# Optimization experiments

Measured on AMD Instinct MI355X. Metric: run time of the kernel, lower is better.

## Reference

```python
import jax, jax.numpy as jnp
import numpy as np

HIDDEN = 1024
NUM_HEADS = 16
HEAD_SIZE = HIDDEN // NUM_HEADS  # 64
SQ, SK, B = 256, 1024, 8


def setup_inputs() -> dict:
    key = jax.random.key(0)
    ks = jax.random.split(key, 8)
    s = 0.02
    return {
        "x": jax.random.normal(ks[0], (SQ, B, HIDDEN), jnp.float32),
        "memory": jax.random.normal(ks[1], (SK, B, HIDDEN), jnp.float32),
        "Wq": jax.random.normal(ks[2], (HIDDEN, HIDDEN), jnp.float32) * s,
        "bq": jax.random.normal(ks[3], (HIDDEN,), jnp.float32) * s,
        "Wkv": jax.random.normal(ks[4], (2 * HIDDEN, HIDDEN), jnp.float32) * s,
        "bkv": jax.random.normal(ks[5], (2 * HIDDEN,), jnp.float32) * s,
        "Wd": jax.random.normal(ks[6], (HIDDEN, HIDDEN), jnp.float32) * s,
        "bd": jax.random.normal(ks[7], (HIDDEN,), jnp.float32) * s,
    }


def reference(x, memory, Wq, bq, Wkv, bkv, Wd, bd):
    # x: (Sq, B, E), memory: (Sk, B, E)  -- sequence-first layout
    Sq, Bb, E = x.shape
    Sk = memory.shape[0]
    H, Dh = NUM_HEADS, HEAD_SIZE

    q = x @ Wq.T + bq            # (Sq, B, E)
    kv = memory @ Wkv.T + bkv    # (Sk, B, 2E)

    # view (..., H, Dh) then composite permute (1,3,0,2):
    # NOTE: the original module's chained permutes put tensors in
    # (batch, head_size, seq, num_heads) layout, so the score matmul
    # contracts over num_heads and head_size acts as the head axis.
    q = q.reshape(Sq, Bb, H, Dh).transpose((1, 3, 0, 2))          # (B, Dh, Sq, H)
    kv = kv.reshape(Sk, Bb, H, 2 * Dh)
    k = kv[..., :Dh].transpose((1, 3, 0, 2))                       # (B, Dh, Sk, H)
    v = kv[..., Dh:].transpose((1, 3, 0, 2))                       # (B, Dh, Sk, H)

    scale = 1.0 / np.sqrt(float(Dh)).astype(np.float32)
    scores = jnp.einsum('bdqh,bdkh->bdqk', q, k) * scale           # (B, Dh, Sq, Sk)
    attn = jax.nn.softmax(scores, axis=-1)
    # attention_dropout omitted (eval mode / p=0)
    ctx = jnp.einsum('bdqk,bdkh->bdqh', attn, v)                   # (B, Dh, Sq, H)

    # transpose(1,2) -> (B, Sq, Dh, H), reshape concatenates Dh-major
    ctx = ctx.transpose((0, 2, 1, 3)).reshape(Bb, Sq, E)
    ctx = ctx.transpose((1, 0, 2))                                 # (Sq, B, E)
    out = ctx @ Wd.T + bd
    # output dropout omitted (eval mode / p=0)
    return out
```

## Files before the change

### kernel.cpp

```cpp
#include <hip/hip_runtime.h>


typedef float f32x4 __attribute__((ext_vector_type(4)));
typedef __bf16 bf16x8 __attribute__((ext_vector_type(8)));
typedef short s16x8 __attribute__((ext_vector_type(8)));
typedef unsigned int u32x2 __attribute__((ext_vector_type(2)));
typedef unsigned int u32x4 __attribute__((ext_vector_type(4)));

__device__ __forceinline__ unsigned short f2bf(float f) {
    unsigned int u = __builtin_bit_cast(unsigned int, f);
    u += 0x7fffu + ((u >> 16) & 1u);
    return (unsigned short)(u >> 16);
}
__device__ __forceinline__ unsigned cvt_pk_bf16(float lo, float hi_) {
    unsigned r;
    asm("v_cvt_pk_bf16_f32 %0, %1, %2" : "=v"(r) : "v"(lo), "v"(hi_));
    return r;
}
__device__ __forceinline__ s16x8 cvt8(float4 a, float4 b) {
    u32x4 r;
    r[0] = cvt_pk_bf16(a.x, a.y); r[1] = cvt_pk_bf16(a.z, a.w);
    r[2] = cvt_pk_bf16(b.x, b.y); r[3] = cvt_pk_bf16(b.z, b.w);
    return __builtin_bit_cast(s16x8, r);
}
__device__ __forceinline__ void gload_lds16(const unsigned short* g,
                                            unsigned short* l) {
    __builtin_amdgcn_global_load_lds(
        (const __attribute__((address_space(1))) void*)g,
        (__attribute__((address_space(3))) void*)l, 16, 0, 0);
}

__global__ void cvt_f32_bf16(const float* __restrict__ src,
                             unsigned short* __restrict__ dst) {
    int i = (blockIdx.x * 256 + threadIdx.x) * 8;
    float4 a = *reinterpret_cast<const float4*>(src + i);
    float4 b = *reinterpret_cast<const float4*>(src + i + 4);
    *reinterpret_cast<s16x8*>(dst + i) = cvt8(a, b);
}

__global__ void cvt_fused4(const float* __restrict__ x,
                           const float* __restrict__ mem,
                           const float* __restrict__ wq,
                           const float* __restrict__ wkv,
                           unsigned short* __restrict__ xb,
                           unsigned short* __restrict__ mb,
                           unsigned short* __restrict__ wqb,
                           unsigned short* __restrict__ wkvb) {
    long t = (long)blockIdx.x * 256 + threadIdx.x;
    const float* src; unsigned short* dst; long off;
    if (t < 262144)                { src = x;   dst = xb;   off = t; }
    else if (t < 262144 + 1048576) { src = mem; dst = mb;   off = t - 262144; }
    else if (t < 1441792)          { src = wq;  dst = wqb;  off = t - 1310720; }
    else                           { src = wkv; dst = wkvb; off = t - 1441792; }
    long i = off * 8;
    float4 a = *reinterpret_cast<const float4*>(src + i);
    float4 b = *reinterpret_cast<const float4*>(src + i + 4);
    *reinterpret_cast<s16x8*>(dst + i) = cvt8(a, b);
}

template <int OUT_BF16>
__global__ __launch_bounds__(256, 2)
void gemm_bt(const unsigned short* __restrict__ A,
             const unsigned short* __restrict__ Bw,
             const float* __restrict__ bias,
             void* __restrict__ Cout,
             int M, int N, int K, float scale) {
    __shared__ unsigned short As[128][64];
    __shared__ unsigned short Bs[128][64];

    const int tid = threadIdx.x;
    const int bm = blockIdx.x, bn = blockIdx.y;
    const int lane = tid & 63;
    const int w = tid >> 6;
    const int wr = w >> 1, wc = w & 1;
    const int l15 = lane & 15, lg = lane >> 4;

    f32x4 acc[4][4] = {};

    for (int k0 = 0; k0 < K; k0 += 64) {
#pragma unroll
        for (int it = 0; it < 8; ++it) {
            const int isB = it >> 2;
            int cbase = ((it & 3) << 8) + w * 64;
            int c = cbase + lane;
            int row = c >> 3, slotp = c & 7;
            int slot = slotp ^ (row & 7);
            const unsigned short* src = isB ? Bw : A;
            int grow = (isB ? bn : bm) * 128 + row;
            const unsigned short* gptr = src + (size_t)grow * K + k0 + slot * 8;
            unsigned short* lptr = (isB ? &Bs[0][0] : &As[0][0]) + cbase * 8;
            gload_lds16(gptr, lptr);
        }
        __syncthreads();

#pragma unroll
        for (int kk = 0; kk < 2; ++kk) {
            bf16x8 afr[4], bfr[4];
#pragma unroll
            for (int mi = 0; mi < 4; ++mi) {
                int row = wr * 64 + mi * 16 + l15;
                int slot = (kk * 4 + lg) ^ (row & 7);
                afr[mi] = *reinterpret_cast<const bf16x8*>(&As[row][slot * 8]);
            }
#pragma unroll
            for (int nj = 0; nj < 4; ++nj) {
                int row = wc * 64 + nj * 16 + l15;
                int slot = (kk * 4 + lg) ^ (row & 7);
                bfr[nj] = *reinterpret_cast<const bf16x8*>(&Bs[row][slot * 8]);
            }
#pragma unroll
            for (int mi = 0; mi < 4; ++mi)
#pragma unroll
                for (int nj = 0; nj < 4; ++nj)
                    acc[mi][nj] = __builtin_amdgcn_mfma_f32_16x16x32_bf16(
                        afr[mi], bfr[nj], acc[mi][nj], 0, 0, 0);
        }
        __syncthreads();
    }

#pragma unroll
    for (int nj = 0; nj < 4; ++nj) {
        int n = bn * 128 + wc * 64 + nj * 16 + l15;
        float bv = bias[n];
#pragma unroll
        for (int mi = 0; mi < 4; ++mi) {
#pragma unroll
            for (int r = 0; r < 4; ++r) {
                int m = bm * 128 + wr * 64 + mi * 16 + lg * 4 + r;
                float val = (acc[mi][nj][r] + bv) * scale;
                if (OUT_BF16)
                    ((unsigned short*)Cout)[(size_t)m * N + n] = f2bf(val);
                else
                    ((float*)Cout)[(size_t)m * N + n] = val;
            }
        }
    }
}

__global__ __launch_bounds__(256, 2)
void transpose_kv(const unsigned short* __restrict__ kvb,
                  unsigned short* __restrict__ Kp,
                  unsigned short* __restrict__ Vp) {
    __shared__ unsigned short Tl[32 * 1024];
    const int b = blockIdx.x, skc = blockIdx.y, dc = blockIdx.z;
    const int tid = threadIdx.x;
    const int sk0 = skc * 32;
#pragma unroll
    for (int it = 0; it < 16; ++it) {
        int c = it * 256 + tid;
        int r = c >> 7, w = c & 127;
        int seg = w >> 2, j = w & 3;
        int col = (seg >> 1) * 128 + (seg & 1) * 64 + dc * 32 + j * 8;
        s16x8 v = *reinterpret_cast<const s16x8*>(
            kvb + (size_t)((sk0 + r) * 8 + b) * 2048 + col);
        *reinterpret_cast<s16x8*>(&Tl[r * 1024 + seg * 32 + j * 8]) = v;
    }
    __syncthreads();
    const int dl = tid >> 3;
#pragma unroll
    for (int it = 0; it < 8; ++it) {
        int sub = it * 8 + (tid & 7);
        int r = sub >> 1, hh = sub & 1;
        s16x8 o;
#pragma unroll
        for (int e = 0; e < 8; ++e) {
            int h = hh * 8 + e;
            o[e] = Tl[r * 1024 + (h * 2) * 32 + dl];
        }
        *reinterpret_cast<s16x8*>(
            Kp + ((size_t)(b * 64 + dc * 32 + dl) * 1024 + sk0 + r) * 16 + hh * 8) = o;
    }
#pragma unroll
    for (int it = 0; it < 8; ++it) {
        int sub = it * 8 + (tid & 7);
        int h = sub >> 2, oct = sub & 3;
        s16x8 o;
#pragma unroll
        for (int e = 0; e < 8; ++e) {
            int r = oct * 8 + e;
            o[e] = Tl[r * 1024 + (h * 2 + 1) * 32 + dl];
        }
        *reinterpret_cast<s16x8*>(
            Vp + ((size_t)(b * 64 + dc * 32 + dl) * 32 + skc) * 512 + h * 32 + oct * 8) = o;
    }
}

__global__ __launch_bounds__(256, 2)
void transpose_q(const unsigned short* __restrict__ qb,
                 unsigned short* __restrict__ Qp) {
    __shared__ unsigned short Tl[32 * 512];
    const int b = blockIdx.x, sqc = blockIdx.y, dc = blockIdx.z;
    const int tid = threadIdx.x;
    const int sq0 = sqc * 32;
#pragma unroll
    for (int it = 0; it < 8; ++it) {
        int c = it * 256 + tid;
        int r = c >> 6, w = c & 63;
        int h = w >> 2, j = w & 3;
        s16x8 v = *reinterpret_cast<const s16x8*>(
            qb + (size_t)((sq0 + r) * 8 + b) * 1024 + h * 64 + dc * 32 + j * 8);
        *reinterpret_cast<s16x8*>(&Tl[r * 512 + h * 32 + j * 8]) = v;
    }
    __syncthreads();
    const int dl = tid >> 3;
#pragma unroll
    for (int it = 0; it < 8; ++it) {
        int sub = it * 8 + (tid & 7);
        int r = sub >> 1, hh = sub & 1;
        s16x8 o;
#pragma unroll
        for (int e = 0; e < 8; ++e)
            o[e] = Tl[r * 512 + (hh * 8 + e) * 32 + dl];
        *reinterpret_cast<s16x8*>(
            Qp + ((size_t)(b * 64 + dc * 32 + dl) * 256 + sq0 + r) * 16 + hh * 8) = o;
    }
}

__global__ __launch_bounds__(256, 4)
void attn_partial(const unsigned short* __restrict__ Qp,
                  const unsigned short* __restrict__ Kp,
                  const unsigned short* __restrict__ Vp,
                  float* __restrict__ ctxp,
                  float* __restrict__ lp) {
    __shared__ alignas(16) unsigned short KsU[64 * 16];
    __shared__ alignas(16) unsigned short VsU[2 * 512];
    __shared__ alignas(16) unsigned short Plds[4][2][16][40];

    const int bdsp = blockIdx.x;
    const int bd = bdsp >> 1, sp = bdsp & 1;
    const int tid = threadIdx.x;
    const int w = tid >> 6, lane = tid & 63;
    const int l15 = lane & 15, lg = lane >> 4, effLg = lg & 1;

    s16x8 zero8 = {};
    const bf16x8 zfr = __builtin_bit_cast(bf16x8, zero8);

    bf16x8 qfr[4];
#pragma unroll
    for (int st = 0; st < 4; ++st) {
        int sq = w * 64 + st * 16 + l15;
        bf16x8 t = *reinterpret_cast<const bf16x8*>(
            Qp + ((size_t)bd * 256 + sq) * 16 + effLg * 8);
        qfr[st] = (lg < 2) ? t : zfr;
    }

    const int li = tid & 127;
    const bool isV = tid >= 128;
    const unsigned short* src =
        (isV ? Vp : Kp) + (size_t)bd * 16384 + sp * 8192 + li * 8;
    unsigned short* dst = (isV ? VsU : KsU) + li * 8;

    f32x4 ctx[4] = {};
    float lq[4] = {0.f, 0.f, 0.f, 0.f};

    s16x8 pfch = *reinterpret_cast<const s16x8*>(src);

    for (int it = 0; it < 8; ++it) {
        *reinterpret_cast<s16x8*>(dst) = pfch;
        __syncthreads();
        if (it < 7) pfch = *reinterpret_cast<const s16x8*>(src + (it + 1) * 1024);

        bf16x8 kf[4];
#pragma unroll
        for (int t4 = 0; t4 < 4; ++t4) {
            bf16x8 t = *reinterpret_cast<const bf16x8*>(
                KsU + (t4 * 16 + l15) * 16 + effLg * 8);
            kf[t4] = (lg < 2) ? t : zfr;
        }
        bf16x8 vf0 = *reinterpret_cast<const bf16x8*>(VsU + l15 * 32 + lg * 8);
        bf16x8 vf1 = *reinterpret_cast<const bf16x8*>(VsU + 512 + l15 * 32 + lg * 8);

#pragma unroll
        for (int st = 0; st < 4; ++st) {
            f32x4 z = {};
            f32x4 s0 = __builtin_amdgcn_mfma_f32_16x16x32_bf16(kf[0], qfr[st], z, 0, 0, 0);
            f32x4 s1 = __builtin_amdgcn_mfma_f32_16x16x32_bf16(kf[1], qfr[st], z, 0, 0, 0);
            f32x4 s2 = __builtin_amdgcn_mfma_f32_16x16x32_bf16(kf[2], qfr[st], z, 0, 0, 0);
            f32x4 s3 = __builtin_amdgcn_mfma_f32_16x16x32_bf16(kf[3], qfr[st], z, 0, 0, 0);

            float p0[4], p1[4], p2[4], p3[4];
#pragma unroll
            for (int r = 0; r < 4; ++r) {
                p0[r] = __expf(s0[r]); p1[r] = __expf(s1[r]);
                p2[r] = __expf(s2[r]); p3[r] = __expf(s3[r]);
            }
            float ps = ((p0[0] + p0[1]) + (p0[2] + p0[3])) +
                       ((p1[0] + p1[1]) + (p1[2] + p1[3])) +
                       ((p2[0] + p2[1]) + (p2[2] + p2[3])) +
                       ((p3[0] + p3[1]) + (p3[2] + p3[3]));
            ps += __shfl_xor(ps, 16);
            ps += __shfl_xor(ps, 32);
            lq[st] += ps;

            u32x2 wA, wB;
            wA[0] = cvt_pk_bf16(p0[0], p0[1]); wA[1] = cvt_pk_bf16(p0[2], p0[3]);
            wB[0] = cvt_pk_bf16(p1[0], p1[1]); wB[1] = cvt_pk_bf16(p1[2], p1[3]);
            *reinterpret_cast<u32x2*>(&Plds[w][0][l15][lg * 4]) = wA;
            *reinterpret_cast<u32x2*>(&Plds[w][0][l15][16 + lg * 4]) = wB;
            u32x2 wC, wD;
            wC[0] = cvt_pk_bf16(p2[0], p2[1]); wC[1] = cvt_pk_bf16(p2[2], p2[3]);
            wD[0] = cvt_pk_bf16(p3[0], p3[1]); wD[1] = cvt_pk_bf16(p3[2], p3[3]);
            *reinterpret_cast<u32x2*>(&Plds[w][1][l15][lg * 4]) = wC;
            *reinterpret_cast<u32x2*>(&Plds[w][1][l15][16 + lg * 4]) = wD;

            bf16x8 pfr0 = *reinterpret_cast<const bf16x8*>(&Plds[w][0][l15][lg * 8]);
            ctx[st] = __builtin_amdgcn_mfma_f32_16x16x32_bf16(pfr0, vf0, ctx[st], 0, 0, 0);
            bf16x8 pfr1 = *reinterpret_cast<const bf16x8*>(&Plds[w][1][l15][lg * 8]);
            ctx[st] = __builtin_amdgcn_mfma_f32_16x16x32_bf16(pfr1, vf1, ctx[st], 0, 0, 0);
        }
        __syncthreads();
    }

#pragma unroll
    for (int st = 0; st < 4; ++st) {
        if (lg == 0)
            lp[(size_t)bdsp * 256 + w * 64 + st * 16 + l15] = lq[st];
#pragma unroll
        for (int r = 0; r < 4; ++r) {
            int sq = w * 64 + st * 16 + lg * 4 + r;
            ctxp[((size_t)bdsp * 256 + sq) * 16 + l15] = ctx[st][r];
        }
    }
}

__global__ __launch_bounds__(256, 8)
void attn_combine(const float* __restrict__ ctxp,
                  const float* __restrict__ lp,
                  unsigned short* __restrict__ ctxb) {
    int idx = blockIdx.x * 256 + threadIdx.x;
    int bd = idx >> 8, sq = idx & 255;
    int b = bd >> 6, d = bd & 63;
    const float* c0 = ctxp + ((size_t)(bd * 2) * 256 + sq) * 16;
    const float* c1 = c0 + 256 * 16;
    float inv = 1.f / (lp[(size_t)(bd * 2) * 256 + sq] +
                       lp[(size_t)(bd * 2 + 1) * 256 + sq]);
    s16x8 o0, o1;
#pragma unroll
    for (int j = 0; j < 2; ++j) {
        float4 a0 = *reinterpret_cast<const float4*>(c0 + j * 8);
        float4 a1 = *reinterpret_cast<const float4*>(c0 + j * 8 + 4);
        float4 b0 = *reinterpret_cast<const float4*>(c1 + j * 8);
        float4 b1 = *reinterpret_cast<const float4*>(c1 + j * 8 + 4);
        s16x8& o = j ? o1 : o0;
        o[0] = (short)f2bf((a0.x + b0.x) * inv);
        o[1] = (short)f2bf((a0.y + b0.y) * inv);
        o[2] = (short)f2bf((a0.z + b0.z) * inv);
        o[3] = (short)f2bf((a0.w + b0.w) * inv);
        o[4] = (short)f2bf((a1.x + b1.x) * inv);
        o[5] = (short)f2bf((a1.y + b1.y) * inv);
        o[6] = (short)f2bf((a1.z + b1.z) * inv);
        o[7] = (short)f2bf((a1.w + b1.w) * inv);
    }
    unsigned short* dst = ctxb + (size_t)(sq * 8 + b) * 1024 + d * 16;
    *reinterpret_cast<s16x8*>(dst) = o0;
    *reinterpret_cast<s16x8*>(dst + 8) = o1;
}

extern "C" void kernel_launch(void* const* d_in, const int* in_sizes, int n_in,
                              void* d_out, int out_size, void* d_ws, size_t ws_size,
                              hipStream_t stream) {
    const float* x   = (const float*)d_in[0];
    const float* mem = (const float*)d_in[1];
    const float* Wq  = (const float*)d_in[2];
    const float* bq  = (const float*)d_in[3];
    const float* Wkv = (const float*)d_in[4];
    const float* bkv = (const float*)d_in[5];
    const float* Wd  = (const float*)d_in[6];
    const float* bd  = (const float*)d_in[7];
    float* out = (float*)d_out;

    const size_t M = 1024 * 1024;
    unsigned short* ws    = (unsigned short*)d_ws;
    unsigned short* qbuf  = ws;
    unsigned short* kvbuf = ws + 2 * M;
    unsigned short* Kp    = ws + 18 * M;
    unsigned short* Vp    = ws + 26 * M;
    unsigned short* xb    = ws + 18 * M;
    unsigned short* mb    = ws + 20 * M;
    unsigned short* wqb   = ws + 28 * M;
    unsigned short* wkvb  = ws + 29 * M;
    unsigned short* ctxb  = ws + 2 * M;
    unsigned short* Qp    = ws + 4 * M;
    unsigned short* wdb   = ws + 6 * M;
    float*          ctxp  = (float*)(ws + 8 * M);
    float*          lp    = (float*)(ws + 17 * M);

    cvt_fused4<<<6656, 256, 0, stream>>>(x, mem, Wq, Wkv, xb, mb, wqb, wkvb);

    gemm_bt<1><<<dim3(2048 / 128, 1024 / 128), 256, 0, stream>>>(
        xb, wqb, bq, qbuf, 2048, 1024, 1024, 0.125f);
    gemm_bt<1><<<dim3(8192 / 128, 2048 / 128), 256, 0, stream>>>(
        mb, wkvb, bkv, kvbuf, 8192, 2048, 1024, 1.0f);

    transpose_kv<<<dim3(8, 32, 2), 256, 0, stream>>>(kvbuf, Kp, Vp);
    transpose_q<<<dim3(8, 8, 2), 256, 0, stream>>>(qbuf, Qp);

    cvt_f32_bf16<<<512, 256, 0, stream>>>(Wd, wdb);

    attn_partial<<<1024, 256, 0, stream>>>(Qp, Kp, Vp, ctxp, lp);
    attn_combine<<<512, 256, 0, stream>>>(ctxp, lp, ctxb);

    gemm_bt<0><<<dim3(2048 / 128, 1024 / 128), 256, 0, stream>>>(
        ctxb, wdb, bd, out, 2048, 1024, 1024, 1.0f);
}
```

Baseline: 150.1 us.

## Fuse attention split-K combine into single pass and stage bf16 GEMM epilogue via LDS

The attention kernel now splits work over query halves instead of key halves, so each block walks the full key sequence and normalizes its own output. This removes the fp32 partial context and sum buffers and the separate combine kernel, along with their global traffic and a launch. Each block now reloads all of K/V while computing half the queries, so K/V reads double. Separately, the bf16 GEMM epilogue writes tiles to shared memory and then stores coalesced 16-byte rows instead of scattered 2-byte stores.

```diff
diff --git a/kernel.cpp b/kernel.cpp
--- a/kernel.cpp
+++ b/kernel.cpp
@@ -65,8 +65,9 @@
              const float* __restrict__ bias,
              void* __restrict__ Cout,
              int M, int N, int K, float scale) {
-    __shared__ unsigned short As[128][64];
-    __shared__ unsigned short Bs[128][64];
+    __shared__ unsigned short U[16384];
+    unsigned short(*As)[64] = (unsigned short(*)[64])U;
+    unsigned short(*Bs)[64] = (unsigned short(*)[64])(U + 8192);
 
     const int tid = threadIdx.x;
     const int bm = blockIdx.x, bn = blockIdx.y;
@@ -118,21 +119,41 @@
         __syncthreads();
     }
 
-#pragma unroll
-    for (int nj = 0; nj < 4; ++nj) {
-        int n = bn * 128 + wc * 64 + nj * 16 + l15;
-        float bv = bias[n];
-#pragma unroll
-        for (int mi = 0; mi < 4; ++mi) {
-#pragma unroll
-            for (int r = 0; r < 4; ++r) {
-                int m = bm * 128 + wr * 64 + mi * 16 + lg * 4 + r;
-                float val = (acc[mi][nj][r] + bv) * scale;
-                if (OUT_BF16)
-                    ((unsigned short*)Cout)[(size_t)m * N + n] = f2bf(val);
-                else
-                    ((float*)Cout)[(size_t)m * N + n] = val;
-            }
+    if (OUT_BF16) {
+        unsigned short(*Cs)[128] = (unsigned short(*)[128])U;
+#pragma unroll
+        for (int nj = 0; nj < 4; ++nj) {
+            int ln = wc * 64 + nj * 16 + l15;
+            float bv = bias[bn * 128 + ln];
+#pragma unroll
+            for (int mi = 0; mi < 4; ++mi)
+#pragma unroll
+                for (int r = 0; r < 4; ++r) {
+                    int lm = wr * 64 + mi * 16 + lg * 4 + r;
+                    Cs[lm][ln] = f2bf((acc[mi][nj][r] + bv) * scale);
+                }
+        }
+        __syncthreads();
+#pragma unroll
+        for (int p = 0; p < 8; ++p) {
+            int c = p * 256 + tid;
+            int row = c >> 4, seg = c & 15;
+            s16x8 v = *reinterpret_cast<const s16x8*>(&Cs[row][seg * 8]);
+            *reinterpret_cast<s16x8*>((unsigned short*)Cout +
+                (size_t)(bm * 128 + row) * N + bn * 128 + seg * 8) = v;
+        }
+    } else {
+#pragma unroll
+        for (int nj = 0; nj < 4; ++nj) {
+            int n = bn * 128 + wc * 64 + nj * 16 + l15;
+            float bv = bias[n];
+#pragma unroll
+            for (int mi = 0; mi < 4; ++mi)
+#pragma unroll
+                for (int r = 0; r < 4; ++r) {
+                    int m = bm * 128 + wr * 64 + mi * 16 + lg * 4 + r;
+                    ((float*)Cout)[(size_t)m * N + n] = (acc[mi][nj][r] + bv) * scale;
+                }
         }
     }
 }
@@ -217,17 +238,17 @@
 }
 
 __global__ __launch_bounds__(256, 4)
-void attn_partial(const unsigned short* __restrict__ Qp,
-                  const unsigned short* __restrict__ Kp,
-                  const unsigned short* __restrict__ Vp,
-                  float* __restrict__ ctxp,
-                  float* __restrict__ lp) {
+void attn_full(const unsigned short* __restrict__ Qp,
+               const unsigned short* __restrict__ Kp,
+               const unsigned short* __restrict__ Vp,
+               unsigned short* __restrict__ ctxb) {
     __shared__ alignas(16) unsigned short KsU[64 * 16];
     __shared__ alignas(16) unsigned short VsU[2 * 512];
     __shared__ alignas(16) unsigned short Plds[4][2][16][40];
 
-    const int bdsp = blockIdx.x;
-    const int bd = bdsp >> 1, sp = bdsp & 1;
+    const int bdh = blockIdx.x;
+    const int bd = bdh >> 1, half = bdh & 1;
+    const int b = bd >> 6, d = bd & 63;
     const int tid = threadIdx.x;
     const int w = tid >> 6, lane = tid & 63;
     const int l15 = lane & 15, lg = lane >> 4, effLg = lg & 1;
@@ -235,10 +256,10 @@
     s16x8 zero8 = {};
     const bf16x8 zfr = __builtin_bit_cast(bf16x8, zero8);
 
-    bf16x8 qfr[4];
-#pragma unroll
-    for (int st = 0; st < 4; ++st) {
-        int sq = w * 64 + st * 16 + l15;
+    bf16x8 qfr[2];
+#pragma unroll
+    for (int st = 0; st < 2; ++st) {
+        int sq = half * 128 + w * 32 + st * 16 + l15;
         bf16x8 t = *reinterpret_cast<const bf16x8*>(
             Qp + ((size_t)bd * 256 + sq) * 16 + effLg * 8);
         qfr[st] = (lg < 2) ? t : zfr;
@@ -246,19 +267,18 @@
 
     const int li = tid & 127;
     const bool isV = tid >= 128;
-    const unsigned short* src =
-        (isV ? Vp : Kp) + (size_t)bd * 16384 + sp * 8192 + li * 8;
+    const unsigned short* src = (isV ? Vp : Kp) + (size_t)bd * 16384 + li * 8;
     unsigned short* dst = (isV ? VsU : KsU) + li * 8;
 
-    f32x4 ctx[4] = {};
-    float lq[4] = {0.f, 0.f, 0.f, 0.f};
+    f32x4 ctx[2] = {};
+    float lq[2] = {0.f, 0.f};
 
     s16x8 pfch = *reinterpret_cast<const s16x8*>(src);
 
-    for (int it = 0; it < 8; ++it) {
+    for (int it = 0; it < 16; ++it) {
         *reinterpret_cast<s16x8*>(dst) = pfch;
         __syncthreads();
-        if (it < 7) pfch = *reinterpret_cast<const s16x8*>(src + (it + 1) * 1024);
+        if (it < 15) pfch = *reinterpret_cast<const s16x8*>(src + (it + 1) * 1024);
 
         bf16x8 kf[4];
 #pragma unroll
@@ -271,7 +291,7 @@
         bf16x8 vf1 = *reinterpret_cast<const bf16x8*>(VsU + 512 + l15 * 32 + lg * 8);
 
 #pragma unroll
-        for (int st = 0; st < 4; ++st) {
+        for (int st = 0; st < 2; ++st) {
             f32x4 z = {};
             f32x4 s0 = __builtin_amdgcn_mfma_f32_16x16x32_bf16(kf[0], qfr[st], z, 0, 0, 0);
             f32x4 s1 = __builtin_amdgcn_mfma_f32_16x16x32_bf16(kf[1], qfr[st], z, 0, 0, 0);
@@ -312,48 +332,16 @@
     }
 
 #pragma unroll
-    for (int st = 0; st < 4; ++st) {
-        if (lg == 0)
-            lp[(size_t)bdsp * 256 + w * 64 + st * 16 + l15] = lq[st];
+    for (int st = 0; st < 2; ++st) {
+        float invown = 1.f / lq[st];
 #pragma unroll
         for (int r = 0; r < 4; ++r) {
-            int sq = w * 64 + st * 16 + lg * 4 + r;
-            ctxp[((size_t)bdsp * 256 + sq) * 16 + l15] = ctx[st][r];
-        }
-    }
-}
-
-__global__ __launch_bounds__(256, 8)
-void attn_combine(const float* __restrict__ ctxp,
-                  const float* __restrict__ lp,
-                  unsigned short* __restrict__ ctxb) {
-    int idx = blockIdx.x * 256 + threadIdx.x;
-    int bd = idx >> 8, sq = idx & 255;
-    int b = bd >> 6, d = bd & 63;
-    const float* c0 = ctxp + ((size_t)(bd * 2) * 256 + sq) * 16;
-    const float* c1 = c0 + 256 * 16;
-    float inv = 1.f / (lp[(size_t)(bd * 2) * 256 + sq] +
-                       lp[(size_t)(bd * 2 + 1) * 256 + sq]);
-    s16x8 o0, o1;
-#pragma unroll
-    for (int j = 0; j < 2; ++j) {
-        float4 a0 = *reinterpret_cast<const float4*>(c0 + j * 8);
-        float4 a1 = *reinterpret_cast<const float4*>(c0 + j * 8 + 4);
-        float4 b0 = *reinterpret_cast<const float4*>(c1 + j * 8);
-        float4 b1 = *reinterpret_cast<const float4*>(c1 + j * 8 + 4);
-        s16x8& o = j ? o1 : o0;
-        o[0] = (short)f2bf((a0.x + b0.x) * inv);
-        o[1] = (short)f2bf((a0.y + b0.y) * inv);
-        o[2] = (short)f2bf((a0.z + b0.z) * inv);
-        o[3] = (short)f2bf((a0.w + b0.w) * inv);
-        o[4] = (short)f2bf((a1.x + b1.x) * inv);
-        o[5] = (short)f2bf((a1.y + b1.y) * inv);
-        o[6] = (short)f2bf((a1.z + b1.z) * inv);
-        o[7] = (short)f2bf((a1.w + b1.w) * inv);
-    }
-    unsigned short* dst = ctxb + (size_t)(sq * 8 + b) * 1024 + d * 16;
-    *reinterpret_cast<s16x8*>(dst) = o0;
-    *reinterpret_cast<s16x8*>(dst + 8) = o1;
+            float inv = __shfl(invown, lg * 4 + r);
+            int sq = half * 128 + w * 32 + st * 16 + lg * 4 + r;
+            ctxb[(size_t)(sq * 8 + b) * 1024 + d * 16 + l15] =
+                f2bf(ctx[st][r] * inv);
+        }
+    }
 }
 
 extern "C" void kernel_launch(void* const* d_in, const int* in_sizes, int n_in,
@@ -382,8 +370,6 @@
     unsigned short* ctxb  = ws + 2 * M;
     unsigned short* Qp    = ws + 4 * M;
     unsigned short* wdb   = ws + 6 * M;
-    float*          ctxp  = (float*)(ws + 8 * M);
-    float*          lp    = (float*)(ws + 17 * M);
 
     cvt_fused4<<<6656, 256, 0, stream>>>(x, mem, Wq, Wkv, xb, mb, wqb, wkvb);
 
@@ -397,8 +383,7 @@
 
     cvt_f32_bf16<<<512, 256, 0, stream>>>(Wd, wdb);
 
-    attn_partial<<<1024, 256, 0, stream>>>(Qp, Kp, Vp, ctxp, lp);
-    attn_combine<<<512, 256, 0, stream>>>(ctxp, lp, ctxb);
+    attn_full<<<1024, 256, 0, stream>>>(Qp, Kp, Vp, ctxb);
 
     gemm_bt<0><<<dim3(2048 / 128, 1024 / 128), 256, 0, stream>>>(
         ctxb, wdb, bd, out, 2048, 1024, 1024, 1.0f);
```

Result: faster. 145.4 us (-3.1%).
